# Kernel optimization log

Measured on AMD Instinct MI355X. Metric: run time of the kernel, lower is better.

Reference implementation:

```python
import jax, jax.numpy as jnp
import numpy as np

S, D, H, DK, DV = 4096, 2048, 16, 128, 128


def setup_inputs() -> dict:
    key = jax.random.key(0)
    ks = jax.random.split(key, 9)
    s = lambda fan_in: 1.0 / np.sqrt(fan_in)
    return {
        "x": jax.random.normal(ks[0], (S, D), dtype=jnp.float32),
        "Wq": jax.random.uniform(ks[1], (H, D, DK), jnp.float32, -s(D), s(D)),
        "bq": jax.random.uniform(ks[2], (H, DK), jnp.float32, -s(D), s(D)),
        "Wk": jax.random.uniform(ks[3], (H, D, DK), jnp.float32, -s(D), s(D)),
        "bk": jax.random.uniform(ks[4], (H, DK), jnp.float32, -s(D), s(D)),
        "Wv": jax.random.uniform(ks[5], (H, D, DV), jnp.float32, -s(D), s(D)),
        "bv": jax.random.uniform(ks[6], (H, DV), jnp.float32, -s(D), s(D)),
        "Wo": jax.random.uniform(ks[7], (H * DV, D), jnp.float32, -s(H * DV), s(H * DV)),
        "bo": jax.random.uniform(ks[8], (D,), jnp.float32, -s(H * DV), s(H * DV)),
    }


def reference(x, Wq, bq, Wk, bk, Wv, bv, Wo, bo):
    # Per-head projections batched over the head axis: [H, S, dk/dv]
    q = jnp.einsum("sd,hdk->hsk", x, Wq) + bq[:, None, :]
    k = jnp.einsum("sd,hdk->hsk", x, Wk) + bk[:, None, :]
    v = jnp.einsum("sd,hdv->hsv", x, Wv) + bv[:, None, :]
    # Scaled dot-product attention per head (mask=None path)
    scores = jnp.einsum("hqk,hsk->hqs", q, k) / jnp.sqrt(jnp.asarray(DK, x.dtype))
    attn = jax.nn.softmax(scores, axis=-1)          # [H, S, S]
    out = jnp.einsum("hqs,hsv->hqv", attn, v)       # [H, S, dv]
    # torch.cat(..., dim=1): interleave heads on feature dim -> [S, H*dv]
    cat = jnp.transpose(out, (1, 0, 2)).reshape(S, H * DV)
    return cat @ Wo + bo
```

## Files before the change

### kernel.cpp

```cpp
#include <hip/hip_runtime.h>
#include <hip/hip_bf16.h>

typedef __attribute__((ext_vector_type(8))) short bhalf8;
typedef __attribute__((ext_vector_type(4))) short bhalf4;
typedef __attribute__((ext_vector_type(4))) float f32x4;
typedef __attribute__((ext_vector_type(16))) float f32x16;
typedef __attribute__((ext_vector_type(4))) unsigned int u32x4;

#define S_SEQ 4096
#define DMODEL 2048
#define NHEAD 16
#define DHEAD 128

__device__ __forceinline__ short f2bf(float f) {
  union { float f; unsigned int u; } v; v.f = f;
  unsigned int r = v.u + 0x7fffu + ((v.u >> 16) & 1u);
  return (short)(r >> 16);
}

__device__ __forceinline__ unsigned pk2(float a, float b) {
  union { __hip_bfloat16 h; unsigned short u; } x, y;
  x.h = __float2bfloat16(a); y.h = __float2bfloat16(b);
  return (unsigned)x.u | ((unsigned)y.u << 16);
}

__global__ __launch_bounds__(256) void k_convert(const float* __restrict__ in,
                                                 short* __restrict__ out, int n4) {
  int i = blockIdx.x * 256 + threadIdx.x;
  if (i >= n4) return;
  f32x4 v = ((const f32x4*)in)[i];
  bhalf4 o;
  o[0] = f2bf(v[0]); o[1] = f2bf(v[1]); o[2] = f2bf(v[2]); o[3] = f2bf(v[3]);
  ((bhalf4*)out)[i] = o;
}

__global__ __launch_bounds__(256) void k_transpose(const float* __restrict__ in,
                                                   short* __restrict__ out, int R, int C) {
  long bs = (long)R * C;
  const float* inp = in + (long)blockIdx.y * bs;
  short* outp = out + (long)blockIdx.y * bs;
  int ct = C >> 6;
  int r0 = (blockIdx.x / ct) << 6;
  int c0 = (blockIdx.x % ct) << 6;
  __shared__ float T[64][65];
  int tid = threadIdx.x;
#pragma unroll
  for (int i = 0; i < 4; i++) {
    int chunk = tid + i * 256;
    int r = chunk >> 4, c = (chunk & 15) << 2;
    f32x4 v = *(const f32x4*)(inp + (long)(r0 + r) * C + c0 + c);
    T[r][c] = v[0]; T[r][c + 1] = v[1]; T[r][c + 2] = v[2]; T[r][c + 3] = v[3];
  }
  __syncthreads();
#pragma unroll
  for (int i = 0; i < 4; i++) {
    int chunk = tid + i * 256;
    int oc = chunk >> 4, o4 = (chunk & 15) << 2;
    bhalf4 o;
    o[0] = f2bf(T[o4][oc]);     o[1] = f2bf(T[o4 + 1][oc]);
    o[2] = f2bf(T[o4 + 2][oc]); o[3] = f2bf(T[o4 + 3][oc]);
    *(bhalf4*)(outp + (long)(c0 + oc) * R + r0 + o4) = o;
  }
}

template <int MODE>
__global__ __launch_bounds__(256) void k_gemm(const short* __restrict__ A, int lda, long a_bs,
                                              const short* __restrict__ Bt, int ldb, long b_bs,
                                              void* __restrict__ Cp, int ldc, long c_bs,
                                              const float* __restrict__ bias, int bias_bs,
                                              float alpha,
                                              int Mtiles, int Ntiles, int K) {
  const int b = blockIdx.y;
  A += (long)b * a_bs;
  Bt += (long)b * b_bs;
  bias += (long)b * bias_bs;
  const int bx = blockIdx.x;
  const int mt = bx / Ntiles, nt = bx % Ntiles;
  const int row0 = mt << 7, col0 = nt << 7;
  const int tid = threadIdx.x;
  const int wave = tid >> 6, lane = tid & 63;
  const int wr = wave >> 1, wc = wave & 1;
  const int lr = lane & 15, lg = lane >> 4;

  __shared__ short As[128][72];
  __shared__ short Bs[128][72];

  f32x4 acc[4][4];
#pragma unroll
  for (int mi = 0; mi < 4; mi++)
#pragma unroll
    for (int ni = 0; ni < 4; ni++) acc[mi][ni] = (f32x4){0.f, 0.f, 0.f, 0.f};

  for (int k0 = 0; k0 < K; k0 += 64) {
    __syncthreads();
#pragma unroll
    for (int i = 0; i < 4; i++) {
      int chunk = tid + i * 256;
      int r = chunk >> 3, c = (chunk & 7) << 3;
      *(bhalf8*)&As[r][c] = *(const bhalf8*)(A + (long)(row0 + r) * lda + k0 + c);
      *(bhalf8*)&Bs[r][c] = *(const bhalf8*)(Bt + (long)(col0 + r) * ldb + k0 + c);
    }
    __syncthreads();
#pragma unroll
    for (int kk = 0; kk < 2; kk++) {
      bhalf8 af[4], bf[4];
#pragma unroll
      for (int mi = 0; mi < 4; mi++)
        af[mi] = *(const bhalf8*)&As[wr * 64 + mi * 16 + lr][kk * 32 + lg * 8];
#pragma unroll
      for (int ni = 0; ni < 4; ni++)
        bf[ni] = *(const bhalf8*)&Bs[wc * 64 + ni * 16 + lr][kk * 32 + lg * 8];
#pragma unroll
      for (int mi = 0; mi < 4; mi++)
#pragma unroll
        for (int ni = 0; ni < 4; ni++)
          acc[mi][ni] = __builtin_amdgcn_mfma_f32_16x16x32_bf16(af[mi], bf[ni], acc[mi][ni], 0, 0, 0);
    }
  }

#pragma unroll
  for (int mi = 0; mi < 4; mi++) {
#pragma unroll
    for (int ni = 0; ni < 4; ni++) {
#pragma unroll
      for (int r = 0; r < 4; r++) {
        int row = row0 + wr * 64 + mi * 16 + lg * 4 + r;
        int col = col0 + wc * 64 + ni * 16 + lr;
        float v = acc[mi][ni][r];
        if (MODE == 0) {
          v = (v + bias[col]) * alpha;
          ((short*)Cp)[(long)b * c_bs + (long)row * ldc + col] = f2bf(v);
        } else if (MODE == 1) {
          v = (v + bias[row]) * alpha;
          ((short*)Cp)[(long)b * c_bs + (long)row * ldc + col] = f2bf(v);
        } else {
          v += bias[col];
          ((float*)Cp)[(long)b * c_bs + (long)row * ldc + col] = v;
        }
      }
    }
  }
}

__global__ __launch_bounds__(256, 2) void k_attn(const short* __restrict__ q,
                                                 const short* __restrict__ k,
                                                 const short* __restrict__ vT,
                                                 short* __restrict__ cat) {
  __shared__ __align__(16) char smem[65536];
  const int wg = blockIdx.x;
  const int wgid = (wg & 7) * 64 + (wg >> 3);
  const int h = wgid >> 5;
  const int q0 = (wgid & 31) << 7;
  const int tid = threadIdx.x;
  const int wave = tid >> 6;
  const int l31 = tid & 31;
  const int hi = (tid >> 5) & 1;
  const int swl = (tid & 7) << 4;

  const long qk_base = (long)h * S_SEQ * DHEAD;
  const long vt_base = (long)h * DHEAD * S_SEQ;

  {
    u32x4 qst[8];
#pragma unroll
    for (int rnd = 0; rnd < 8; rnd++) {
      int o = rnd * 4096 + tid * 16;
      int row = o >> 8, col = o & 255;
      qst[rnd] = *(const u32x4*)(q + qk_base + (long)(q0 + row) * DHEAD + (col >> 1));
    }
#pragma unroll
    for (int rnd = 0; rnd < 8; rnd++) {
      int o = rnd * 4096 + tid * 16;
      int row = o >> 8, col = o & 255;
      *(u32x4*)(smem + row * 256 + (col ^ ((row & 7) << 4))) = qst[rnd];
    }
  }
  __syncthreads();
  bhalf8 qf[8];
#pragma unroll
  for (int kc = 0; kc < 8; kc++) {
    int row = wave * 32 + l31;
    qf[kc] = *(const bhalf8*)(smem + row * 256 + ((kc * 32 + hi * 16) ^ swl));
  }
  __syncthreads();

  f32x16 accO[4];
#pragma unroll
  for (int d = 0; d < 4; d++)
#pragma unroll
    for (int r = 0; r < 16; r++) accO[d][r] = 0.f;
  float m_run = -1e30f, l_part = 0.f;

  u32x4 st[8];
  auto load_tile = [&](int kv0) {
#pragma unroll
    for (int rnd = 0; rnd < 4; rnd++) {
      int o = rnd * 4096 + tid * 16;
      int row = o >> 8, col = o & 255;
      st[rnd] = *(const u32x4*)(k + qk_base + (long)(kv0 + row) * DHEAD + (col >> 1));
    }
#pragma unroll
    for (int rnd = 0; rnd < 4; rnd++) {
      int o = rnd * 4096 + tid * 16;
      int row = o >> 7, col = o & 127;
      st[4 + rnd] = *(const u32x4*)(vT + vt_base + (long)row * S_SEQ + kv0 + (col >> 1));
    }
  };
  auto write_tile = [&](char* buf) {
#pragma unroll
    for (int rnd = 0; rnd < 4; rnd++) {
      int o = rnd * 4096 + tid * 16;
      int row = o >> 8, col = o & 255;
      *(u32x4*)(buf + row * 256 + (col ^ ((row & 7) << 4))) = st[rnd];
    }
#pragma unroll
    for (int rnd = 0; rnd < 4; rnd++) {
      int o = rnd * 4096 + tid * 16;
      int row = o >> 7, col = o & 127;
      *(u32x4*)(buf + 16384 + row * 128 + (col ^ ((row & 7) << 4))) = st[4 + rnd];
    }
  };

  load_tile(0);
  write_tile(smem);
  load_tile(64);
  __syncthreads();

  const int NT = S_SEQ / 64;
  for (int t = 0; t < NT; t++) {
    char* buf = smem + (t & 1) * 32768;

    f32x16 accS[2];
#pragma unroll
    for (int kvb = 0; kvb < 2; kvb++)
#pragma unroll
      for (int r = 0; r < 16; r++) accS[kvb][r] = 0.f;

    __builtin_amdgcn_s_setprio(1);
#pragma unroll
    for (int kvb = 0; kvb < 2; kvb++) {
      int row = kvb * 32 + l31;
#pragma unroll
      for (int kc = 0; kc < 8; kc++) {
        bhalf8 kf = *(const bhalf8*)(buf + row * 256 + ((kc * 32 + hi * 16) ^ swl));
        accS[kvb] = __builtin_amdgcn_mfma_f32_32x32x16_bf16(kf, qf[kc], accS[kvb], 0, 0, 0);
      }
    }
    __builtin_amdgcn_s_setprio(0);

    float mx[8];
#pragma unroll
    for (int g = 0; g < 8; g++) {
      const int kvb = g >> 2, b4 = (g & 3) * 4;
      mx[g] = fmaxf(fmaxf(accS[kvb][b4], accS[kvb][b4 + 1]),
                    fmaxf(accS[kvb][b4 + 2], accS[kvb][b4 + 3]));
    }
    float mc = fmaxf(fmaxf(fmaxf(mx[0], mx[1]), fmaxf(mx[2], mx[3])),
                     fmaxf(fmaxf(mx[4], mx[5]), fmaxf(mx[6], mx[7])));
    mc = fmaxf(mc, __shfl_xor(mc, 32));

    if (!__all(mc <= m_run + 8.f)) {
      float mn = fmaxf(m_run, mc);
      float corr = __builtin_amdgcn_exp2f(m_run - mn);
      m_run = mn;
      l_part *= corr;
#pragma unroll
      for (int d = 0; d < 4; d++)
#pragma unroll
        for (int r = 0; r < 16; r++) accO[d][r] *= corr;
    }

    unsigned pk[2][4][2];
#pragma unroll
    for (int kvb = 0; kvb < 2; kvb++)
#pragma unroll
      for (int g = 0; g < 4; g++) {
        float p0 = __builtin_amdgcn_exp2f(accS[kvb][4 * g + 0] - m_run);
        float p1 = __builtin_amdgcn_exp2f(accS[kvb][4 * g + 1] - m_run);
        float p2 = __builtin_amdgcn_exp2f(accS[kvb][4 * g + 2] - m_run);
        float p3 = __builtin_amdgcn_exp2f(accS[kvb][4 * g + 3] - m_run);
        l_part += (p0 + p1) + (p2 + p3);
        pk[kvb][g][0] = pk2(p0, p1);
        pk[kvb][g][1] = pk2(p2, p3);
      }

    bhalf8 pa[4];
#pragma unroll
    for (int kvb = 0; kvb < 2; kvb++)
#pragma unroll
      for (int c1 = 0; c1 < 2; c1++) {
        unsigned a0 = pk[kvb][2 * c1][0],     a1 = pk[kvb][2 * c1][1];
        unsigned b0 = pk[kvb][2 * c1 + 1][0], b1 = pk[kvb][2 * c1 + 1][1];
        unsigned s0a = (unsigned)__shfl_xor((int)a0, 32);
        unsigned s1a = (unsigned)__shfl_xor((int)a1, 32);
        unsigned s0b = (unsigned)__shfl_xor((int)b0, 32);
        unsigned s1b = (unsigned)__shfl_xor((int)b1, 32);
        union { unsigned u[4]; bhalf8 v; } cvt;
        cvt.u[0] = hi ? s0b : a0;
        cvt.u[1] = hi ? s1b : a1;
        cvt.u[2] = hi ? b0 : s0a;
        cvt.u[3] = hi ? b1 : s1a;
        pa[kvb * 2 + c1] = cvt.v;
      }

    __builtin_amdgcn_s_setprio(1);
#pragma unroll
    for (int d = 0; d < 4; d++) {
      int row = d * 32 + l31;
#pragma unroll
      for (int c = 0; c < 4; c++) {
        bhalf8 vf = *(const bhalf8*)(buf + 16384 + row * 128 + ((c * 32 + hi * 16) ^ swl));
        accO[d] = __builtin_amdgcn_mfma_f32_32x32x16_bf16(vf, pa[c], accO[d], 0, 0, 0);
      }
    }
    __builtin_amdgcn_s_setprio(0);

    if (t + 1 < NT) write_tile(smem + ((t + 1) & 1) * 32768);
    __syncthreads();
    if (t + 2 < NT) load_tile((t + 2) * 64);
  }

  float l_tot = l_part + __shfl_xor(l_part, 32);
  float inv = 1.f / l_tot;
  long rowbase = (long)(q0 + wave * 32 + l31) * DMODEL + h * DHEAD;
#pragma unroll
  for (int d = 0; d < 4; d++)
#pragma unroll
    for (int rg = 0; rg < 4; rg++) {
      bhalf4 ov;
#pragma unroll
      for (int i = 0; i < 4; i++) ov[i] = f2bf(accO[d][rg * 4 + i] * inv);
      *(bhalf4*)(cat + rowbase + d * 32 + rg * 8 + hi * 4) = ov;
    }
}

extern "C" void kernel_launch(void* const* d_in, const int* in_sizes, int n_in,
                              void* d_out, int out_size, void* d_ws, size_t ws_size,
                              hipStream_t stream) {
  const float* x  = (const float*)d_in[0];
  const float* Wq = (const float*)d_in[1];
  const float* bq = (const float*)d_in[2];
  const float* Wk = (const float*)d_in[3];
  const float* bk = (const float*)d_in[4];
  const float* Wv = (const float*)d_in[5];
  const float* bv = (const float*)d_in[6];
  const float* Wo = (const float*)d_in[7];
  const float* bo = (const float*)d_in[8];
  float* out = (float*)d_out;

  short* x_bf   = (short*)d_ws;
  short* Wqt    = x_bf  + (long)S_SEQ * DMODEL;
  short* Wkt    = Wqt   + (long)NHEAD * DHEAD * DMODEL;
  short* Wvt    = Wkt   + (long)NHEAD * DHEAD * DMODEL;
  short* Wot    = Wvt   + (long)NHEAD * DHEAD * DMODEL;
  short* q_bf   = Wot   + (long)DMODEL * DMODEL;
  short* k_bf   = q_bf  + (long)NHEAD * S_SEQ * DHEAD;
  short* vT_bf  = k_bf  + (long)NHEAD * S_SEQ * DHEAD;
  short* cat_bf = vT_bf + (long)NHEAD * DHEAD * S_SEQ;

  dim3 blk(256);

  k_convert<<<dim3((S_SEQ * DMODEL / 4 + 255) / 256), blk, 0, stream>>>(x, x_bf, S_SEQ * DMODEL / 4);

  k_transpose<<<dim3((DMODEL / 64) * (DHEAD / 64), NHEAD), blk, 0, stream>>>(Wq, Wqt, DMODEL, DHEAD);
  k_transpose<<<dim3((DMODEL / 64) * (DHEAD / 64), NHEAD), blk, 0, stream>>>(Wk, Wkt, DMODEL, DHEAD);
  k_transpose<<<dim3((DMODEL / 64) * (DHEAD / 64), NHEAD), blk, 0, stream>>>(Wv, Wvt, DMODEL, DHEAD);
  k_transpose<<<dim3((DMODEL / 64) * (DMODEL / 64), 1), blk, 0, stream>>>(Wo, Wot, DMODEL, DMODEL);

  const float alpha_q = 0.08838834764831845f * 1.4426950408889634f;

  k_gemm<0><<<dim3(32, NHEAD), blk, 0, stream>>>(x_bf, DMODEL, 0L,
                                                 Wqt, DMODEL, (long)DHEAD * DMODEL,
                                                 q_bf, DHEAD, (long)S_SEQ * DHEAD,
                                                 bq, DHEAD, alpha_q, 32, 1, DMODEL);
  k_gemm<0><<<dim3(32, NHEAD), blk, 0, stream>>>(x_bf, DMODEL, 0L,
                                                 Wkt, DMODEL, (long)DHEAD * DMODEL,
                                                 k_bf, DHEAD, (long)S_SEQ * DHEAD,
                                                 bk, DHEAD, 1.0f, 32, 1, DMODEL);
  k_gemm<1><<<dim3(32, NHEAD), blk, 0, stream>>>(Wvt, DMODEL, (long)DHEAD * DMODEL,
                                                 x_bf, DMODEL, 0L,
                                                 vT_bf, S_SEQ, (long)DHEAD * S_SEQ,
                                                 bv, DHEAD, 1.0f, 1, 32, DMODEL);

  k_attn<<<dim3(512), blk, 0, stream>>>(q_bf, k_bf, vT_bf, cat_bf);

  k_gemm<2><<<dim3(32 * 16, 1), blk, 0, stream>>>(cat_bf, DMODEL, 0L,
                                                  Wot, DMODEL, 0L,
                                                  out, DMODEL, 0L,
                                                  bo, 0, 1.0f, 32, 16, DMODEL);
}
```

Before: 378.5 us.

## Use 512-thread attention blocks covering 256 queries to share K/V tiles

The attention kernel now launches 256 workgroups of 512 threads (8 waves), each handling 256 query rows instead of 128. Each K/V tile loaded into shared memory is reused by twice as many waves, and each thread loads half as much data per tile. This halves global K/V traffic per query. In exchange there are fewer workgroups (256 on the GPU) and larger barriers, and the launch bounds of 512 threads with 4 blocks requested may constrain registers per thread.

```diff
diff --git a/kernel.cpp b/kernel.cpp
--- a/kernel.cpp
+++ b/kernel.cpp
@@ -142,15 +142,15 @@
   }
 }
 
-__global__ __launch_bounds__(256, 2) void k_attn(const short* __restrict__ q,
+__global__ __launch_bounds__(512, 4) void k_attn(const short* __restrict__ q,
                                                  const short* __restrict__ k,
                                                  const short* __restrict__ vT,
                                                  short* __restrict__ cat) {
   __shared__ __align__(16) char smem[65536];
   const int wg = blockIdx.x;
-  const int wgid = (wg & 7) * 64 + (wg >> 3);
-  const int h = wgid >> 5;
-  const int q0 = (wgid & 31) << 7;
+  const int wgid = (wg & 7) * 32 + (wg >> 3);
+  const int h = wgid >> 4;
+  const int q0 = (wgid & 15) << 8;
   const int tid = threadIdx.x;
   const int wave = tid >> 6;
   const int l31 = tid & 31;
@@ -160,19 +160,20 @@
   const long qk_base = (long)h * S_SEQ * DHEAD;
   const long vt_base = (long)h * DHEAD * S_SEQ;
 
-  {
-    u32x4 qst[8];
-#pragma unroll
-    for (int rnd = 0; rnd < 8; rnd++) {
-      int o = rnd * 4096 + tid * 16;
+#pragma unroll
+  for (int g = 0; g < 2; g++) {
+    u32x4 qst[4];
+#pragma unroll
+    for (int r = 0; r < 4; r++) {
+      int o = (g * 4 + r) * 8192 + tid * 16;
       int row = o >> 8, col = o & 255;
-      qst[rnd] = *(const u32x4*)(q + qk_base + (long)(q0 + row) * DHEAD + (col >> 1));
-    }
-#pragma unroll
-    for (int rnd = 0; rnd < 8; rnd++) {
-      int o = rnd * 4096 + tid * 16;
+      qst[r] = *(const u32x4*)(q + qk_base + (long)(q0 + row) * DHEAD + (col >> 1));
+    }
+#pragma unroll
+    for (int r = 0; r < 4; r++) {
+      int o = (g * 4 + r) * 8192 + tid * 16;
       int row = o >> 8, col = o & 255;
-      *(u32x4*)(smem + row * 256 + (col ^ ((row & 7) << 4))) = qst[rnd];
+      *(u32x4*)(smem + row * 256 + (col ^ ((row & 7) << 4))) = qst[r];
     }
   }
   __syncthreads();
@@ -191,33 +192,33 @@
     for (int r = 0; r < 16; r++) accO[d][r] = 0.f;
   float m_run = -1e30f, l_part = 0.f;
 
-  u32x4 st[8];
+  u32x4 st[4];
   auto load_tile = [&](int kv0) {
 #pragma unroll
-    for (int rnd = 0; rnd < 4; rnd++) {
-      int o = rnd * 4096 + tid * 16;
+    for (int r2 = 0; r2 < 2; r2++) {
+      int o = r2 * 8192 + tid * 16;
       int row = o >> 8, col = o & 255;
-      st[rnd] = *(const u32x4*)(k + qk_base + (long)(kv0 + row) * DHEAD + (col >> 1));
-    }
-#pragma unroll
-    for (int rnd = 0; rnd < 4; rnd++) {
-      int o = rnd * 4096 + tid * 16;
+      st[r2] = *(const u32x4*)(k + qk_base + (long)(kv0 + row) * DHEAD + (col >> 1));
+    }
+#pragma unroll
+    for (int r2 = 0; r2 < 2; r2++) {
+      int o = r2 * 8192 + tid * 16;
       int row = o >> 7, col = o & 127;
-      st[4 + rnd] = *(const u32x4*)(vT + vt_base + (long)row * S_SEQ + kv0 + (col >> 1));
+      st[2 + r2] = *(const u32x4*)(vT + vt_base + (long)row * S_SEQ + kv0 + (col >> 1));
     }
   };
   auto write_tile = [&](char* buf) {
 #pragma unroll
-    for (int rnd = 0; rnd < 4; rnd++) {
-      int o = rnd * 4096 + tid * 16;
+    for (int r2 = 0; r2 < 2; r2++) {
+      int o = r2 * 8192 + tid * 16;
       int row = o >> 8, col = o & 255;
-      *(u32x4*)(buf + row * 256 + (col ^ ((row & 7) << 4))) = st[rnd];
-    }
-#pragma unroll
-    for (int rnd = 0; rnd < 4; rnd++) {
-      int o = rnd * 4096 + tid * 16;
+      *(u32x4*)(buf + row * 256 + (col ^ ((row & 7) << 4))) = st[r2];
+    }
+#pragma unroll
+    for (int r2 = 0; r2 < 2; r2++) {
+      int o = r2 * 8192 + tid * 16;
       int row = o >> 7, col = o & 127;
-      *(u32x4*)(buf + 16384 + row * 128 + (col ^ ((row & 7) << 4))) = st[4 + rnd];
+      *(u32x4*)(buf + 16384 + row * 128 + (col ^ ((row & 7) << 4))) = st[2 + r2];
     }
   };
 
@@ -382,7 +383,7 @@
                                                  vT_bf, S_SEQ, (long)DHEAD * S_SEQ,
                                                  bv, DHEAD, 1.0f, 1, 32, DMODEL);
 
-  k_attn<<<dim3(512), blk, 0, stream>>>(q_bf, k_bf, vT_bf, cat_bf);
+  k_attn<<<dim3(256), dim3(512), 0, stream>>>(q_bf, k_bf, vT_bf, cat_bf);
 
   k_gemm<2><<<dim3(32 * 16, 1), blk, 0, stream>>>(cat_bf, DMODEL, 0L,
                                                   Wot, DMODEL, 0L,
```

Result: slower. 829.4 us (+119.1%).
